# Performance work log

Measured on AMD Instinct MI355X. Metric: run time of the kernel, lower is better.

## Reference

```python
import jax, jax.numpy as jnp
import numpy as np

D_MODEL = 2048
DOWN = 512
UP = 1024
NUM_HEADS = 16
ROPE_DIM = 64
BS = 16
SEQ = 512
BASE = 10000.0
HEAD_DIM = D_MODEL // NUM_HEADS          # 128 (used only in the softmax scale)
V_HEAD_DIM = UP // NUM_HEADS             # 64


def _linear(x, W, b):
    # torch nn.Linear: y = x @ W.T + b, W shape (out, in)
    return x @ W.T + b


def _rope(x, num_heads, rope_dim):
    # Faithful to source RotaryEmbedding, including the swapped sin/cos caches:
    #   cos_pos = sin(pos*theta), sin_pos = cos(pos*theta)
    bs, L, _ = x.shape
    q = x.reshape(bs, L, num_heads, rope_dim).transpose(0, 2, 1, 3)  # (bs,h,L,d)
    theta = 1.0 / (BASE ** (jnp.arange(0, rope_dim, 2, dtype=jnp.float32) / rope_dim))
    ang = jnp.arange(L, dtype=jnp.float32)[:, None] * theta[None, :]   # (L, d/2)
    cos_pos = jnp.repeat(jnp.sin(ang), 2, axis=-1)  # (L, d) -- source quirk
    sin_pos = jnp.repeat(jnp.cos(ang), 2, axis=-1)
    q2 = jnp.stack([-q[..., 1::2], q[..., ::2]], axis=-1).reshape(bs, num_heads, L, rope_dim)
    return q * cos_pos + q2 * sin_pos


def setup_inputs() -> dict:
    key = jax.random.key(0)
    ks = jax.random.split(key, 18)
    s = 0.02
    d = {
        "h": jax.random.normal(ks[0], (BS, SEQ, D_MODEL), jnp.float32),
        "W_down_kv": jax.random.normal(ks[1], (DOWN, D_MODEL), jnp.float32) * s,
        "b_down_kv": jnp.zeros((DOWN,), jnp.float32),
        "W_up_k": jax.random.normal(ks[2], (UP, DOWN), jnp.float32) * s,
        "b_up_k": jnp.zeros((UP,), jnp.float32),
        "W_up_v": jax.random.normal(ks[3], (UP, DOWN), jnp.float32) * s,
        "b_up_v": jnp.zeros((UP,), jnp.float32),
        "W_down_q": jax.random.normal(ks[4], (DOWN, D_MODEL), jnp.float32) * s,
        "b_down_q": jnp.zeros((DOWN,), jnp.float32),
        "W_up_q": jax.random.normal(ks[5], (UP, DOWN), jnp.float32) * s,
        "b_up_q": jnp.zeros((UP,), jnp.float32),
        "W_qr": jax.random.normal(ks[6], (ROPE_DIM * NUM_HEADS, DOWN), jnp.float32) * s,
        "b_qr": jnp.zeros((ROPE_DIM * NUM_HEADS,), jnp.float32),
        "W_kr": jax.random.normal(ks[7], (ROPE_DIM, D_MODEL), jnp.float32) * s,
        "b_kr": jnp.zeros((ROPE_DIM,), jnp.float32),
        "W_fc": jax.random.normal(ks[8], (D_MODEL, NUM_HEADS * V_HEAD_DIM), jnp.float32) * s,
        "b_fc": jnp.zeros((D_MODEL,), jnp.float32),
    }
    return d


def reference(h, W_down_kv, b_down_kv, W_up_k, b_up_k, W_up_v, b_up_v,
              W_down_q, b_down_q, W_up_q, b_up_q, W_qr, b_qr,
              W_kr, b_kr, W_fc, b_fc):
    bs, L, _ = h.shape
    # low-rank KV path
    c_kv = _linear(h, W_down_kv, b_down_kv)             # (bs,L,down)
    k_c = _linear(c_kv, W_up_k, b_up_k)                 # (bs,L,up)
    v_c = _linear(c_kv, W_up_v, b_up_v)                 # (bs,L,up)
    # low-rank Q path
    c_q = _linear(h, W_down_q, b_down_q)                # (bs,L,down)
    q_c = _linear(c_q, W_up_q, b_up_q)                  # (bs,L,up)
    # rope (decoupled) path
    q_r = _rope(_linear(c_q, W_qr, b_qr), NUM_HEADS, ROPE_DIM)  # (bs,H,L,rope)
    k_r = _rope(_linear(h, W_kr, b_kr), 1, ROPE_DIM)            # (bs,1,L,rope)

    q_c = q_c.reshape(bs, L, NUM_HEADS, -1).transpose(0, 2, 1, 3)  # (bs,H,L,64)
    q = jnp.concatenate([q_c, q_r], axis=-1)                        # (bs,H,L,128)
    k_c = k_c.reshape(bs, L, NUM_HEADS, -1).transpose(0, 2, 1, 3)
    k_r = jnp.broadcast_to(k_r, (bs, NUM_HEADS, L, ROPE_DIM))       # shared across heads
    k = jnp.concatenate([k_c, k_r], axis=-1)

    scale = 1.0 / jnp.sqrt(jnp.float32(HEAD_DIM + ROPE_DIM))  # sqrt(192), per source
    scores = jnp.einsum('bhqd,bhkd->bhqk', q, k) * scale
    attn = jax.nn.softmax(scores, axis=-1)  # dropout is identity in eval mode

    v = v_c.reshape(bs, L, NUM_HEADS, V_HEAD_DIM).transpose(0, 2, 1, 3)
    out = jnp.einsum('bhqk,bhkd->bhqd', attn, v)
    out = out.transpose(0, 2, 1, 3).reshape(bs, L, -1)   # (bs,L,H*v_head_dim)
    return _linear(out, W_fc, b_fc)                      # (bs,L,d_model)
```

## Files before the change

### kernel.cpp

```cpp
#include <hip/hip_runtime.h>
#include <hip/hip_bf16.h>

typedef __bf16 bf16x8 __attribute__((ext_vector_type(8)));
typedef float f32x4 __attribute__((ext_vector_type(4)));
using u16 = unsigned short;
using u32 = unsigned int;

__device__ __forceinline__ float bf2f(u16 v) {
    unsigned int u = (unsigned int)v << 16;
    float f; __builtin_memcpy(&f, &u, 4); return f;
}
__device__ __forceinline__ u16 f2bf(float f) {
    unsigned int u; __builtin_memcpy(&u, &f, 4);
    u += 0x7FFFu + ((u >> 16) & 1u);
    return (u16)(u >> 16);
}

struct Cvt9 {
    const float* src[9];
    u16* dst[9];
    int end[9];
};
__global__ __launch_bounds__(256) void cvt_all(Cvt9 d, int total)
{
    int c = blockIdx.x * 256 + threadIdx.x;
    if (c >= total) return;
    int seg = 0;
    while (c >= d.end[seg]) ++seg;
    int local = c - (seg ? d.end[seg - 1] : 0);
    const float* s = d.src[seg] + (size_t)local * 8;
    float4 f0 = *(const float4*)s;
    float4 f1 = *(const float4*)(s + 4);
    u16 tmp[8] = { f2bf(f0.x), f2bf(f0.y), f2bf(f0.z), f2bf(f0.w),
                   f2bf(f1.x), f2bf(f1.y), f2bf(f1.z), f2bf(f1.w) };
    *(uint4*)(d.dst[seg] + (size_t)local * 8) = *(const uint4*)tmp;
}

struct Cpy7 {
    const float* src[7];
    float* dst[7];
    int end[7];
};
__global__ __launch_bounds__(256) void copy_f32(Cpy7 d, int total)
{
    int c = blockIdx.x * 256 + threadIdx.x;
    if (c >= total) return;
    int seg = 0;
    while (c >= d.end[seg]) ++seg;
    int local = c - (seg ? d.end[seg - 1] : 0);
    d.dst[seg][local] = d.src[seg][local];
}

template<bool CF>
__global__ __launch_bounds__(256) void gemm_v3(
    const u16* __restrict__ A0, const u16* __restrict__ B0, void* __restrict__ C0, const float* __restrict__ e0,
    const u16* __restrict__ A1, const u16* __restrict__ B1, void* __restrict__ C1, const float* __restrict__ e1,
    int ysplit, int lda, int ldb, int ldc, int N, int K)
{
    __shared__ __align__(16) u16 As[128 * 64];
    __shared__ __align__(16) u16 Bs[128 * 64];

    const int t = threadIdx.x;
    const int lane = t & 63;
    const int w = t >> 6;
    const int wm = w >> 1, wn = w & 1;
    const int l16 = lane & 15, quad = lane >> 4;
    const int m0 = blockIdx.x * 128;

    const u16* A; const u16* B; void* Cv; const float* bias; int yl;
    if ((int)blockIdx.y < ysplit) { A = A0; B = B0; Cv = C0; bias = e0; yl = blockIdx.y; }
    else                          { A = A1; B = B1; Cv = C1; bias = e1; yl = blockIdx.y - ysplit; }
    const int n0 = yl * 128;

    const int rowi = lane >> 3;
    const int gc   = (lane & 7) ^ rowi;

    f32x4 acc[4][4];
#pragma unroll
    for (int i = 0; i < 4; ++i)
#pragma unroll
        for (int j = 0; j < 4; ++j) acc[i][j] = (f32x4){0.f, 0.f, 0.f, 0.f};

    for (int k0 = 0; k0 < K; k0 += 64) {
        __syncthreads();
#pragma unroll
        for (int i = 0; i < 4; ++i) {
            const int rr = w * 32 + i * 8;
            const u16* ga = A + (size_t)(m0 + rr + rowi) * lda + k0 + gc * 8;
            __builtin_amdgcn_global_load_lds(
                (const __attribute__((address_space(1))) u32*)ga,
                (__attribute__((address_space(3))) u32*)&As[rr * 64], 16, 0, 0);
            const u16* gb = B + (size_t)(n0 + rr + rowi) * ldb + k0 + gc * 8;
            __builtin_amdgcn_global_load_lds(
                (const __attribute__((address_space(1))) u32*)gb,
                (__attribute__((address_space(3))) u32*)&Bs[rr * 64], 16, 0, 0);
        }
        __syncthreads();

#pragma unroll
        for (int kk = 0; kk < 2; ++kk) {
            const int cc = (((kk << 2) + quad) ^ (l16 & 7)) << 3;
            bf16x8 af[4], bfr[4];
#pragma unroll
            for (int i = 0; i < 4; ++i)
                af[i] = *(const bf16x8*)&As[(wm * 64 + i * 16 + l16) * 64 + cc];
#pragma unroll
            for (int j = 0; j < 4; ++j)
                bfr[j] = *(const bf16x8*)&Bs[(wn * 64 + j * 16 + l16) * 64 + cc];
#pragma unroll
            for (int i = 0; i < 4; ++i)
#pragma unroll
                for (int j = 0; j < 4; ++j)
                    acc[i][j] = __builtin_amdgcn_mfma_f32_16x16x32_bf16(af[i], bfr[j], acc[i][j], 0, 0, 0);
        }
    }

#pragma unroll
    for (int j = 0; j < 4; ++j) {
        int col = n0 + wn * 64 + j * 16 + l16;
        if (col >= N) continue;
        float bv = bias[col];
#pragma unroll
        for (int i = 0; i < 4; ++i) {
#pragma unroll
            for (int r = 0; r < 4; ++r) {
                int row = m0 + wm * 64 + i * 16 + quad * 4 + r;
                float v = acc[i][j][r] + bv;
                if (CF) ((float*)Cv)[(size_t)row * ldc + col] = v;
                else    ((u16*)Cv)[(size_t)row * ldc + col] = f2bf(v);
            }
        }
    }
}

__global__ void rope_inplace(u16* __restrict__ buf, int ld, int col0, int ppr, int total)
{
    int idx = blockIdx.x * 256 + threadIdx.x;
    if (idx >= total) return;
    int row = idx / ppr;
    int pi  = idx - row * ppr;
    int grp = pi >> 5;
    int i   = pi & 31;
    int pos = row & 511;
    float theta = __expf(-(float)i * 0.2878231366242558f);
    float ang = (float)pos * theta;
    float s = sinf(ang), c = cosf(ang);
    size_t base = (size_t)row * ld + col0 + grp * 64 + 2 * i;
    float x0 = bf2f(buf[base]);
    float x1 = bf2f(buf[base + 1]);
    buf[base]     = f2bf(x0 * s - x1 * c);
    buf[base + 1] = f2bf(x1 * s + x0 * c);
}

__global__ __launch_bounds__(256) void attn_kernel(
    const u16* __restrict__ q_src,
    const u16* __restrict__ kv_src,
    const u16* __restrict__ kr_src,
    u16* __restrict__ o_dst, int ldo)
{
    __shared__ __align__(16) u16 Ks[64 * 136];
    __shared__ __align__(16) u16 Vt[64 * 72];
    __shared__ __align__(16) u16 Ps[64 * 72];

    const int t = threadIdx.x;
    const int lane = t & 63;
    const int w = t >> 6;
    const int l16 = lane & 15, quad = lane >> 4;
    const int h  = blockIdx.x;
    const int b  = blockIdx.y;
    const int qt = blockIdx.z;
    const int qrow0 = b * 512 + qt * 64;
    const int krow_base = b * 512;

    bf16x8 aq[4];
    {
        const u16* qrow = q_src + (size_t)(qrow0 + w * 16 + l16) * 2048;
#pragma unroll
        for (int ks = 0; ks < 4; ++ks) {
            int col = ks * 32 + quad * 8;
            const u16* src = (col < 64) ? qrow + h * 64 + col
                                        : qrow + 1024 + h * 64 + (col - 64);
            aq[ks] = *(const bf16x8*)src;
        }
    }

    const int colK = (t & 15) * 8;
    const int r0k  = t >> 4;
    const u16* kbase; int kstr;
    if (colK < 64) { kbase = kv_src + h * 64 + colK;        kstr = 2048; }
    else           { kbase = kr_src + 1024 + (colK - 64);   kstr = 1088; }
    u16* kw = &Ks[r0k * 136 + colK];

    const int v00 = (t & 7) * 8;
    const int r0v = t >> 3;
    const u16* vbase = kv_src + 1024 + h * 64 + v00;
    const int rotA = (r0v + v00) & 63;
    const int rotB = (r0v + 32 + v00) & 63;
    u16* vwA = &Vt[v00 * 72 + rotA];
    u16* vwB = &Vt[v00 * 72 + rotB];

    auto LOADT = [&](int krow0, uint4& K0, uint4& K1, uint4& K2, uint4& K3,
                     uint4& V0, uint4& V1) {
        K0 = *(const uint4*)(kbase + (size_t)(krow0 + r0k     ) * kstr);
        K1 = *(const uint4*)(kbase + (size_t)(krow0 + r0k + 16) * kstr);
        K2 = *(const uint4*)(kbase + (size_t)(krow0 + r0k + 32) * kstr);
        K3 = *(const uint4*)(kbase + (size_t)(krow0 + r0k + 48) * kstr);
        V0 = *(const uint4*)(vbase + (size_t)(krow0 + r0v     ) * 2048);
        V1 = *(const uint4*)(vbase + (size_t)(krow0 + r0v + 32) * 2048);
    };
    auto WRITET = [&](const uint4& K0, const uint4& K1, const uint4& K2, const uint4& K3,
                      const uint4& V0, const uint4& V1) {
        *(uint4*)(kw)            = K0;
        *(uint4*)(kw + 16 * 136) = K1;
        *(uint4*)(kw + 32 * 136) = K2;
        *(uint4*)(kw + 48 * 136) = K3;
        u16 ta[8], tb[8];
        __builtin_memcpy(ta, &V0, 16);
        __builtin_memcpy(tb, &V1, 16);
#pragma unroll
        for (int j2 = 0; j2 < 8; ++j2) { vwA[j2 * 72] = ta[j2]; vwB[j2 * 72] = tb[j2]; }
    };

    float m2[4], l_run[4];
    f32x4 o[4];
#pragma unroll
    for (int r = 0; r < 4; ++r) { m2[r] = -1e30f; l_run[r] = 0.f; }
#pragma unroll
    for (int n = 0; n < 4; ++n) o[n] = (f32x4){0.f, 0.f, 0.f, 0.f};

    const float C = 0.10411756f;
    const int Rp = (64 - (quad << 4)) & 48;
    const int Rr = (64 - ((l16 >> 2) << 4)) & 48;

    uint4 kA0, kA1, kA2, kA3, vA0, vA1;
    uint4 kB0, kB1, kB2, kB3, vB0, vB1;
    LOADT(krow_base, kA0, kA1, kA2, kA3, vA0, vA1);

    for (int kt = 0; kt < 8; ++kt) {
        __syncthreads();
        if ((kt & 1) == 0) {
            WRITET(kA0, kA1, kA2, kA3, vA0, vA1);
            if (kt < 7) LOADT(krow_base + (kt + 1) * 64, kB0, kB1, kB2, kB3, vB0, vB1);
        } else {
            WRITET(kB0, kB1, kB2, kB3, vB0, vB1);
            if (kt < 7) LOADT(krow_base + (kt + 1) * 64, kA0, kA1, kA2, kA3, vA0, vA1);
        }
        __syncthreads();

        f32x4 s[4];
#pragma unroll
        for (int n = 0; n < 4; ++n) s[n] = (f32x4){0.f, 0.f, 0.f, 0.f};
#pragma unroll
        for (int ks = 0; ks < 4; ++ks) {
#pragma unroll
            for (int n = 0; n < 4; ++n) {
                bf16x8 bk = *(const bf16x8*)&Ks[(n * 16 + l16) * 136 + ks * 32 + quad * 8];
                s[n] = __builtin_amdgcn_mfma_f32_16x16x32_bf16(aq[ks], bk, s[n], 0, 0, 0);
            }
        }

        float mx[4], alpha[4], rs[4];
#pragma unroll
        for (int r = 0; r < 4; ++r)
            mx[r] = fmaxf(fmaxf(s[0][r], s[1][r]), fmaxf(s[2][r], s[3][r]));
#pragma unroll
        for (int d = 1; d < 16; d <<= 1)
#pragma unroll
            for (int r = 0; r < 4; ++r)
                mx[r] = fmaxf(mx[r], __shfl_xor(mx[r], d));
#pragma unroll
        for (int r = 0; r < 4; ++r) {
            float mnew = fmaxf(m2[r], mx[r] * C);
            alpha[r] = __builtin_amdgcn_exp2f(m2[r] - mnew);
            m2[r] = mnew;
            rs[r] = 0.f;
#pragma unroll
            for (int n = 0; n < 4; ++n) {
                float pv = __builtin_amdgcn_exp2f(__builtin_fmaf(s[n][r], C, -mnew));
                s[n][r] = pv;
                rs[r] += pv;
            }
        }
#pragma unroll
        for (int d = 1; d < 16; d <<= 1)
#pragma unroll
            for (int r = 0; r < 4; ++r)
                rs[r] += __shfl_xor(rs[r], d);
#pragma unroll
        for (int r = 0; r < 4; ++r) {
            l_run[r] = l_run[r] * alpha[r] + rs[r];
#pragma unroll
            for (int n = 0; n < 4; ++n) o[n][r] *= alpha[r];
        }

#pragma unroll
        for (int n = 0; n < 4; ++n) {
            int pc = (n * 16 + l16 + Rp) & 63;
#pragma unroll
            for (int r = 0; r < 4; ++r)
                Ps[(w * 16 + quad * 4 + r) * 72 + pc] = f2bf(s[n][r]);
        }

#pragma unroll
        for (int kk = 0; kk < 2; ++kk) {
            bf16x8 ap = *(const bf16x8*)&Ps[(w * 16 + l16) * 72 + ((kk * 32 + quad * 8 + Rr) & 63)];
#pragma unroll
            for (int n = 0; n < 4; ++n) {
                bf16x8 bv = *(const bf16x8*)&Vt[(n * 16 + l16) * 72
                              + ((kk * 32 + quad * 8 + n * 16 + (l16 & 8)) & 63)];
                o[n] = __builtin_amdgcn_mfma_f32_16x16x32_bf16(ap, bv, o[n], 0, 0, 0);
            }
        }
    }

#pragma unroll
    for (int r = 0; r < 4; ++r) {
        float inv = 1.0f / l_run[r];
        int row = qrow0 + w * 16 + quad * 4 + r;
#pragma unroll
        for (int n = 0; n < 4; ++n) {
            int col = h * 64 + n * 16 + l16;
            o_dst[(size_t)row * ldo + col] = f2bf(o[n][r] * inv);
        }
    }
}

extern "C" void kernel_launch(void* const* d_in, const int* in_sizes, int n_in,
                              void* d_out, int out_size, void* d_ws, size_t ws_size,
                              hipStream_t stream)
{
    const float* h    = (const float*)d_in[0];
    const float* Wdkv = (const float*)d_in[1];
    const float* bdkv = (const float*)d_in[2];
    const float* Wuk  = (const float*)d_in[3];
    const float* buk  = (const float*)d_in[4];
    const float* Wuv  = (const float*)d_in[5];
    const float* buv  = (const float*)d_in[6];
    const float* Wdq  = (const float*)d_in[7];
    const float* bdq  = (const float*)d_in[8];
    const float* Wuq  = (const float*)d_in[9];
    const float* buq  = (const float*)d_in[10];
    const float* Wqr  = (const float*)d_in[11];
    const float* bqr  = (const float*)d_in[12];
    const float* Wkr  = (const float*)d_in[13];
    const float* bkr  = (const float*)d_in[14];
    const float* Wfc  = (const float*)d_in[15];
    const float* bfc  = (const float*)d_in[16];

    char* ws = (char*)d_ws;
    u16* out1   = (u16*)ws;
    u16* hbf    = (u16*)(ws + 17825792);
    u16* out2a  = hbf;
    u16* out2b  = (u16*)(ws + 51380224);
    u16* w1     = (u16*)(ws + 84934656);
    u16* w2a    = (u16*)(ws + 89653248);
    u16* w2b    = (u16*)(ws + 91750400);
    u16* wfc    = (u16*)(ws + 93847552);
    float* bias_s1 = (float*)(ws + 98041856);
    float* bias_2  = (float*)(ws + 98046208);

    Cvt9 cd;
    const float* srcs[9] = { h, Wdkv, Wdq, Wkr, Wuk, Wuv, Wuq, Wqr, Wfc };
    u16* dsts[9] = { hbf, w1, w1 + 512 * 2048, w1 + 1024 * 2048,
                     w2a, w2a + 1024 * 512, w2b, w2b + 1024 * 512, wfc };
    int cnts[9] = { 2097152, 131072, 131072, 16384, 65536, 65536, 65536, 65536, 262144 };
    int acc2 = 0;
    for (int i = 0; i < 9; ++i) { cd.src[i] = srcs[i]; cd.dst[i] = dsts[i]; acc2 += cnts[i]; cd.end[i] = acc2; }
    cvt_all<<<(acc2 + 255) / 256, 256, 0, stream>>>(cd, acc2);
    hipMemsetAsync(w1 + 1088 * 2048, 0, 64 * 2048 * sizeof(u16), stream);

    Cpy7 bc;
    const float* bs[7] = { bdkv, bdq, bkr, buk, buv, buq, bqr };
    float* bd[7] = { bias_s1, bias_s1 + 512, bias_s1 + 1024,
                     bias_2, bias_2 + 1024, bias_2 + 2048, bias_2 + 3072 };
    int bn[7] = { 512, 512, 64, 1024, 1024, 1024, 1024 };
    int bacc = 0;
    for (int i = 0; i < 7; ++i) { bc.src[i] = bs[i]; bc.dst[i] = bd[i]; bacc += bn[i]; bc.end[i] = bacc; }
    copy_f32<<<(bacc + 255) / 256, 256, 0, stream>>>(bc, bacc);

    gemm_v3<false><<<dim3(64, 9), 256, 0, stream>>>(
        hbf, w1, out1, bias_s1,
        hbf, w1, out1, bias_s1, 9, 2048, 2048, 1088, 1088, 2048);
    rope_inplace<<<1024, 256, 0, stream>>>(out1, 1088, 1024, 32, 8192 * 32);

    gemm_v3<false><<<dim3(64, 32), 256, 0, stream>>>(
        out1,       w2a, out2a, bias_2,
        out1 + 512, w2b, out2b, bias_2 + 2048, 16, 1088, 512, 2048, 2048, 512);
    rope_inplace<<<16384, 256, 0, stream>>>(out2b, 2048, 1024, 512, 8192 * 512);

    attn_kernel<<<dim3(16, 16, 8), 256, 0, stream>>>(out2b, out2a, out1, out1, 1088);

    gemm_v3<true><<<dim3(64, 16), 256, 0, stream>>>(
        out1, wfc, d_out, bfc,
        out1, wfc, d_out, bfc, 16, 1088, 1024, 2048, 2048, 1024);
}
```

Baseline: 448.0 us.

## Double-buffer GEMM LDS tiles with async prefetch and remap attention blocks per XCD

The GEMM now uses two 128x32 LDS buffers per operand. It issues the global-to-LDS loads for the next K-slice before computing the current one, and uses partial vmcnt waits and raw s_barrier in place of a full __syncthreads pair per 64-wide K step. This is meant to overlap memory latency with MFMA work, at the cost of twice as many loop iterations and a new swizzle. The attention launch becomes a 1D grid whose index is remapped so blocks sharing the same (batch, head) K/V panel land on the same XCD, aiming to improve L2 reuse. Its barriers are also replaced with explicit lgkmcnt waits.

```diff
diff --git a/kernel.cpp b/kernel.cpp
--- a/kernel.cpp
+++ b/kernel.cpp
@@ -52,13 +52,13 @@
 }
 
 template<bool CF>
-__global__ __launch_bounds__(256) void gemm_v3(
+__global__ __launch_bounds__(256) void gemm_v4(
     const u16* __restrict__ A0, const u16* __restrict__ B0, void* __restrict__ C0, const float* __restrict__ e0,
     const u16* __restrict__ A1, const u16* __restrict__ B1, void* __restrict__ C1, const float* __restrict__ e1,
     int ysplit, int lda, int ldb, int ldc, int N, int K)
 {
-    __shared__ __align__(16) u16 As[128 * 64];
-    __shared__ __align__(16) u16 Bs[128 * 64];
+    __shared__ __align__(16) u16 As[2][128 * 32];
+    __shared__ __align__(16) u16 Bs[2][128 * 32];
 
     const int t = threadIdx.x;
     const int lane = t & 63;
@@ -72,8 +72,10 @@
     else                          { A = A1; B = B1; Cv = C1; bias = e1; yl = blockIdx.y - ysplit; }
     const int n0 = yl * 128;
 
-    const int rowi = lane >> 3;
-    const int gc   = (lane & 7) ^ rowi;
+    const int sub  = lane >> 2;
+    const int slot = lane & 3;
+    const int agc  = slot ^ ((sub >> 1) & 3);
+    const int sfr  = (l16 >> 1) & 3;
 
     f32x4 acc[4][4];
 #pragma unroll
@@ -81,38 +83,52 @@
 #pragma unroll
         for (int j = 0; j < 4; ++j) acc[i][j] = (f32x4){0.f, 0.f, 0.f, 0.f};
 
-    for (int k0 = 0; k0 < K; k0 += 64) {
-        __syncthreads();
-#pragma unroll
-        for (int i = 0; i < 4; ++i) {
-            const int rr = w * 32 + i * 8;
-            const u16* ga = A + (size_t)(m0 + rr + rowi) * lda + k0 + gc * 8;
+    auto STAGE = [&](int buf, int k0) {
+#pragma unroll
+        for (int c = 0; c < 2; ++c) {
+            const int rr = w * 32 + c * 16;
+            const u16* ga = A + (size_t)(m0 + rr + sub) * lda + k0 + agc * 8;
             __builtin_amdgcn_global_load_lds(
                 (const __attribute__((address_space(1))) u32*)ga,
-                (__attribute__((address_space(3))) u32*)&As[rr * 64], 16, 0, 0);
-            const u16* gb = B + (size_t)(n0 + rr + rowi) * ldb + k0 + gc * 8;
+                (__attribute__((address_space(3))) u32*)&As[buf][rr * 32], 16, 0, 0);
+            const u16* gb = B + (size_t)(n0 + rr + sub) * ldb + k0 + agc * 8;
             __builtin_amdgcn_global_load_lds(
                 (const __attribute__((address_space(1))) u32*)gb,
-                (__attribute__((address_space(3))) u32*)&Bs[rr * 64], 16, 0, 0);
-        }
-        __syncthreads();
-
-#pragma unroll
-        for (int kk = 0; kk < 2; ++kk) {
-            const int cc = (((kk << 2) + quad) ^ (l16 & 7)) << 3;
-            bf16x8 af[4], bfr[4];
-#pragma unroll
-            for (int i = 0; i < 4; ++i)
-                af[i] = *(const bf16x8*)&As[(wm * 64 + i * 16 + l16) * 64 + cc];
+                (__attribute__((address_space(3))) u32*)&Bs[buf][rr * 32], 16, 0, 0);
+        }
+    };
+
+    const int nt = K >> 5;
+    STAGE(0, 0);
+    for (int tt = 0; tt < nt; ++tt) {
+        const int cur = tt & 1;
+        if (tt + 1 < nt) {
+            STAGE(cur ^ 1, (tt + 1) << 5);
+            asm volatile("s_waitcnt vmcnt(4)");
+        } else {
+            asm volatile("s_waitcnt vmcnt(0)");
+        }
+        __builtin_amdgcn_sched_barrier(0);
+        __builtin_amdgcn_s_barrier();
+        __builtin_amdgcn_sched_barrier(0);
+
+        const u16* Ab = As[cur];
+        const u16* Bb = Bs[cur];
+        bf16x8 af[4], bfr[4];
+#pragma unroll
+        for (int i = 0; i < 4; ++i)
+            af[i] = *(const bf16x8*)&Ab[(wm * 64 + i * 16 + l16) * 32 + (quad ^ sfr) * 8];
+#pragma unroll
+        for (int j = 0; j < 4; ++j)
+            bfr[j] = *(const bf16x8*)&Bb[(wn * 64 + j * 16 + l16) * 32 + (quad ^ sfr) * 8];
+#pragma unroll
+        for (int i = 0; i < 4; ++i)
 #pragma unroll
             for (int j = 0; j < 4; ++j)
-                bfr[j] = *(const bf16x8*)&Bs[(wn * 64 + j * 16 + l16) * 64 + cc];
-#pragma unroll
-            for (int i = 0; i < 4; ++i)
-#pragma unroll
-                for (int j = 0; j < 4; ++j)
-                    acc[i][j] = __builtin_amdgcn_mfma_f32_16x16x32_bf16(af[i], bfr[j], acc[i][j], 0, 0, 0);
-        }
+                acc[i][j] = __builtin_amdgcn_mfma_f32_16x16x32_bf16(af[i], bfr[j], acc[i][j], 0, 0, 0);
+
+        __builtin_amdgcn_s_barrier();
+        __builtin_amdgcn_sched_barrier(0);
     }
 
 #pragma unroll
@@ -166,9 +182,13 @@
     const int lane = t & 63;
     const int w = t >> 6;
     const int l16 = lane & 15, quad = lane >> 4;
-    const int h  = blockIdx.x;
-    const int b  = blockIdx.y;
-    const int qt = blockIdx.z;
+
+    const int id   = blockIdx.x;
+    const int xcd  = id & 7;
+    const int qt   = (id >> 3) & 7;
+    const int panel = xcd + ((id >> 6) << 3);
+    const int h = panel & 15;
+    const int b = panel >> 4;
     const int qrow0 = b * 512 + qt * 64;
     const int krow_base = b * 512;
 
@@ -237,7 +257,8 @@
     LOADT(krow_base, kA0, kA1, kA2, kA3, vA0, vA1);
 
     for (int kt = 0; kt < 8; ++kt) {
-        __syncthreads();
+        __builtin_amdgcn_s_barrier();
+        __builtin_amdgcn_sched_barrier(0);
         if ((kt & 1) == 0) {
             WRITET(kA0, kA1, kA2, kA3, vA0, vA1);
             if (kt < 7) LOADT(krow_base + (kt + 1) * 64, kB0, kB1, kB2, kB3, vB0, vB1);
@@ -245,7 +266,10 @@
             WRITET(kB0, kB1, kB2, kB3, vB0, vB1);
             if (kt < 7) LOADT(krow_base + (kt + 1) * 64, kA0, kA1, kA2, kA3, vA0, vA1);
         }
-        __syncthreads();
+        asm volatile("s_waitcnt lgkmcnt(0)");
+        __builtin_amdgcn_sched_barrier(0);
+        __builtin_amdgcn_s_barrier();
+        __builtin_amdgcn_sched_barrier(0);
 
         f32x4 s[4];
 #pragma unroll
@@ -378,19 +402,19 @@
     for (int i = 0; i < 7; ++i) { bc.src[i] = bs[i]; bc.dst[i] = bd[i]; bacc += bn[i]; bc.end[i] = bacc; }
     copy_f32<<<(bacc + 255) / 256, 256, 0, stream>>>(bc, bacc);
 
-    gemm_v3<false><<<dim3(64, 9), 256, 0, stream>>>(
+    gemm_v4<false><<<dim3(64, 9), 256, 0, stream>>>(
         hbf, w1, out1, bias_s1,
         hbf, w1, out1, bias_s1, 9, 2048, 2048, 1088, 1088, 2048);
     rope_inplace<<<1024, 256, 0, stream>>>(out1, 1088, 1024, 32, 8192 * 32);
 
-    gemm_v3<false><<<dim3(64, 32), 256, 0, stream>>>(
+    gemm_v4<false><<<dim3(64, 32), 256, 0, stream>>>(
         out1,       w2a, out2a, bias_2,
         out1 + 512, w2b, out2b, bias_2 + 2048, 16, 1088, 512, 2048, 2048, 512);
     rope_inplace<<<16384, 256, 0, stream>>>(out2b, 2048, 1024, 512, 8192 * 512);
 
-    attn_kernel<<<dim3(16, 16, 8), 256, 0, stream>>>(out2b, out2a, out1, out1, 1088);
-
-    gemm_v3<true><<<dim3(64, 16), 256, 0, stream>>>(
+    attn_kernel<<<2048, 256, 0, stream>>>(out2b, out2a, out1, out1, 1088);
+
+    gemm_v4<true><<<dim3(64, 16), 256, 0, stream>>>(
         out1, wfc, d_out, bfc,
         out1, wfc, d_out, bfc, 16, 1088, 1024, 2048, 2048, 1024);
 }
```

New measurement: 431.1 us. 3.8% less time.
